# Kernel optimization log

Measured on AMD Instinct MI355X. Metric: run time of the kernel, lower is better.

## Reference

```python
import jax, jax.numpy as jnp
import numpy as np

B, T, C, H, W = 2, 2048, 2048, 16, 512
D = C // H  # head_dim = 128

def setup_inputs() -> dict:
    key = jax.random.key(0)
    k1, k2, k3 = jax.random.split(key, 3)
    x = jax.random.normal(k1, (B, T, C), dtype=jnp.float32)
    w_attn = jax.random.normal(k2, (C, 3 * C), dtype=jnp.float32) * 0.02
    w_proj = jax.random.normal(k3, (C, C), dtype=jnp.float32) * 0.02
    # standard RoPE tables: [T, D] with halves repeated
    inv_freq = 1.0 / (10000.0 ** (jnp.arange(0, D, 2, dtype=jnp.float32) / D))
    freqs = jnp.outer(jnp.arange(T, dtype=jnp.float32), inv_freq)  # [T, D/2]
    emb = jnp.concatenate([freqs, freqs], axis=-1)  # [T, D]
    return {"x": x, "freqs_cos": jnp.cos(emb), "freqs_sin": jnp.sin(emb),
            "w_attn": w_attn, "w_proj": w_proj}

def _rotate_half(t):
    return jnp.concatenate([-t[..., D // 2:], t[..., :D // 2]], axis=-1)

def reference(x, freqs_cos, freqs_sin, w_attn, w_proj):
    qkv = x @ w_attn  # [B,T,3C]
    q, k, v = jnp.split(qkv, 3, axis=-1)
    # [B,T,C] -> [B,H,T,D]
    q = q.reshape(B, T, H, D).transpose(0, 2, 1, 3)
    k = k.reshape(B, T, H, D).transpose(0, 2, 1, 3)
    v = v.reshape(B, T, H, D).transpose(0, 2, 1, 3)
    cos = freqs_cos[None, None, :, :]  # [1,1,T,D]
    sin = freqs_sin[None, None, :, :]
    q = q * cos + _rotate_half(q) * sin
    k = k * cos + _rotate_half(k) * sin
    scores = jnp.einsum('bhqd,bhkd->bhqk', q, k) / jnp.sqrt(jnp.float32(D))
    i = jnp.arange(T)[:, None]
    j = jnp.arange(T)[None, :]
    band = (j <= i) & (j > i - W)  # causal sliding window of width W
    scores = jnp.where(band[None, None, :, :], scores, -jnp.inf)
    att = jax.nn.softmax(scores, axis=-1)
    y = jnp.einsum('bhqk,bhkd->bhqd', att, v)
    y = y.transpose(0, 2, 1, 3).reshape(B, T, C)
    return y @ w_proj
```

## Files before the change

### kernel.cpp

```cpp
#include <hip/hip_runtime.h>
#include <stdint.h>

#define B_ 2
#define T_ 2048
#define C_ 2048
#define H_ 16
#define D_ 128
#define W_ 512
#define M_ (B_*T_)
#define N1_ (3*C_)

typedef short bf16x8 __attribute__((ext_vector_type(8)));
typedef unsigned short u16x8 __attribute__((ext_vector_type(8)));
typedef float f32x4 __attribute__((ext_vector_type(4)));

#define SGB __builtin_amdgcn_sched_group_barrier

__device__ __forceinline__ unsigned short f2bf(float f) {
  union { float f; unsigned u; } v; v.f = f;
  unsigned r = v.u + 0x7fffu + ((v.u >> 16) & 1u);
  return (unsigned short)(r >> 16);
}
__device__ __forceinline__ float bf2f(unsigned short b) {
  union { unsigned u; float f; } v; v.u = ((unsigned)b) << 16;
  return v.f;
}

__device__ __forceinline__ void gload_lds16(const void* g, void* l) {
  __builtin_amdgcn_global_load_lds((const __attribute__((address_space(1))) void*)g,
                                   (__attribute__((address_space(3))) void*)l, 16, 0, 0);
}

__global__ void k_cvt(const float* __restrict__ s, unsigned short* __restrict__ d, int n) {
  int i = (blockIdx.x * blockDim.x + threadIdx.x) * 8;
  if (i >= n) return;
  float4 a = *(const float4*)(s + i);
  float4 b = *(const float4*)(s + i + 4);
  u16x8 o;
  o[0]=f2bf(a.x); o[1]=f2bf(a.y); o[2]=f2bf(a.z); o[3]=f2bf(a.w);
  o[4]=f2bf(b.x); o[5]=f2bf(b.y); o[6]=f2bf(b.z); o[7]=f2bf(b.w);
  *(u16x8*)(d + i) = o;
}

__global__ void k_tcvt(const float* __restrict__ s, unsigned short* __restrict__ d, int R, int Cc) {
  __shared__ float tile[32][33];
  int c0 = blockIdx.x * 32, r0 = blockIdx.y * 32;
  int tx = threadIdx.x & 31, ty = threadIdx.x >> 5;
  #pragma unroll
  for (int j = 0; j < 32; j += 8) tile[ty + j][tx] = s[(size_t)(r0 + ty + j) * Cc + c0 + tx];
  __syncthreads();
  #pragma unroll
  for (int j = 0; j < 32; j += 8) d[(size_t)(c0 + ty + j) * R + r0 + tx] = f2bf(tile[tx][ty + j]);
}

template<int ROWS>
__device__ __forceinline__ void stage_half(const unsigned short* __restrict__ gbase,
                                           int row0, int K, int kt, int kh,
                                           unsigned short* region, int tid, int sw) {
  const char* gsrc = (const char*)(gbase + (size_t)row0 * K + kt * 64 + kh * 32);
  {
    int o = tid * 16, s = o ^ sw;
    gload_lds16(gsrc + (size_t)(s >> 6) * (K * 2) + (s & 63), (char*)region + o);
  }
  if (ROWS == 256) {
    int o = (512 + tid) * 16, s = o ^ sw;
    gload_lds16(gsrc + (size_t)(s >> 6) * (K * 2) + (s & 63), (char*)region + o);
  }
}

template<int BN, bool F32OUT>
__global__ __launch_bounds__(512, 2) void k_gemm8(const unsigned short* __restrict__ A,
                                                  const unsigned short* __restrict__ Bt,
                                                  void* __restrict__ Cp,
                                                  int Ntot, int K) {
  constexpr int NBF = BN / 64;
  constexpr int BROWS = (BN == 256) ? 256 : 128;
  __shared__ unsigned short As[2][2][256 * 32];
  __shared__ unsigned short Bs[2][2][BN * 32];
  const int tid = threadIdx.x, lane = tid & 63, wv = tid >> 6;
  const int wm = wv >> 2, wn = wv & 3;
  const int lr = lane & 15, lg = lane >> 4;
  const int sw = tid & 32;
  const int fofs = lr * 64 + ((lg * 16) ^ ((lr & 8) << 2));
  const int aoff = wm * 128 * 64 + fofs;
  const int boff = wn * (BN / 4) * 64 + fofs;

  const int nwg = gridDim.x;
  const int nbx = Ntot / BN;
  const int q = nwg >> 3, r = nwg & 7;
  const int xcd = blockIdx.x & 7, off = blockIdx.x >> 3;
  const int bid = (xcd < r ? xcd * (q + 1) : r * (q + 1) + (xcd - r) * q) + off;
  const int bm0 = (bid / nbx) << 8;
  const int bn0 = (bid % nbx) * BN;

  f32x4 acc[8][NBF];
  #pragma unroll
  for (int i = 0; i < 8; ++i)
    #pragma unroll
    for (int j = 0; j < NBF; ++j)
      #pragma unroll
      for (int e = 0; e < 4; ++e) acc[i][j][e] = 0.f;

  const int NT = K >> 6;

  stage_half<256  >(A,  bm0, K, 0, 0, As[0][0], tid, sw);
  stage_half<BROWS>(Bt, bn0, K, 0, 0, Bs[0][0], tid, sw);
  stage_half<BROWS>(Bt, bn0, K, 0, 1, Bs[0][1], tid, sw);
  stage_half<256  >(A,  bm0, K, 0, 1, As[0][1], tid, sw);
  stage_half<BROWS>(Bt, bn0, K, 1, 0, Bs[1][0], tid, sw);
  stage_half<256  >(A,  bm0, K, 1, 0, As[1][0], tid, sw);
  stage_half<BROWS>(Bt, bn0, K, 1, 1, Bs[1][1], tid, sw);
  asm volatile("s_waitcnt vmcnt(4)" ::: "memory");
  __builtin_amdgcn_s_barrier();

  bf16x8 Xa[4], Xb[NBF], Ya[4];
  #pragma unroll
  for (int j = 0; j < NBF; ++j) Xb[j] = *(const bf16x8*)((const char*)Bs[0][0] + boff + j * 1024);
  #pragma unroll
  for (int i = 0; i < 4; ++i) Xa[i] = *(const bf16x8*)((const char*)As[0][0] + aoff + i * 1024);

  #pragma unroll 2
  for (int t = 0; t < NT; ++t) {
    const int p = t & 1;
    const char* Ar0 = (const char*)As[p][0];
    const char* Ar1 = (const char*)As[p][1];
    const char* Br1 = (const char*)Bs[p][1];
    const char* ArN = (const char*)As[p ^ 1][0];
    const char* BrN = (const char*)Bs[p ^ 1][0];

    asm volatile("s_waitcnt lgkmcnt(0)" ::: "memory");
    __builtin_amdgcn_sched_barrier(0);
    __builtin_amdgcn_s_setprio(1);
    #pragma unroll
    for (int j = 0; j < NBF; ++j)
      #pragma unroll
      for (int i = 0; i < 4; ++i)
        acc[i][j] = __builtin_amdgcn_mfma_f32_16x16x32_bf16(Xa[i], Xb[j], acc[i][j], 0, 0, 0);
    #pragma unroll
    for (int i = 0; i < 4; ++i) Ya[i] = *(const bf16x8*)(Ar0 + aoff + (i + 4) * 1024);
    #pragma unroll
    for (int g = 0; g < 2 * NBF; ++g) { SGB(0x8, 2, 0); if (g < 4) SGB(0x100, 1, 0); }
    __builtin_amdgcn_s_setprio(0);
    if (t + 1 < NT) stage_half<256>(A, bm0, K, t + 1, 1, As[p ^ 1][1], tid, sw);
    __builtin_amdgcn_s_barrier();

    asm volatile("s_waitcnt lgkmcnt(0)" ::: "memory");
    __builtin_amdgcn_sched_barrier(0);
    __builtin_amdgcn_s_setprio(1);
    #pragma unroll
    for (int j = 0; j < NBF; ++j)
      #pragma unroll
      for (int i = 0; i < 4; ++i)
        acc[i + 4][j] = __builtin_amdgcn_mfma_f32_16x16x32_bf16(Ya[i], Xb[j], acc[i + 4][j], 0, 0, 0);
    #pragma unroll
    for (int i = 0; i < 4; ++i) Xa[i] = *(const bf16x8*)(Ar1 + aoff + i * 1024);
    #pragma unroll
    for (int j = 0; j < NBF; ++j) Xb[j] = *(const bf16x8*)(Br1 + boff + j * 1024);
    #pragma unroll
    for (int g = 0; g < 2 * NBF; ++g) { SGB(0x8, 2, 0); if (g < 4 + NBF) SGB(0x100, 1, 0); }
    if (4 + NBF > 2 * NBF) SGB(0x100, 4 + NBF - 2 * NBF, 0);
    __builtin_amdgcn_s_setprio(0);
    if (t + 2 < NT) stage_half<BROWS>(Bt, bn0, K, t + 2, 0, Bs[p][0], tid, sw);
    __builtin_amdgcn_s_barrier();

    asm volatile("s_waitcnt lgkmcnt(0)" ::: "memory");
    __builtin_amdgcn_sched_barrier(0);
    __builtin_amdgcn_s_setprio(1);
    #pragma unroll
    for (int j = 0; j < NBF; ++j)
      #pragma unroll
      for (int i = 0; i < 4; ++i)
        acc[i][j] = __builtin_amdgcn_mfma_f32_16x16x32_bf16(Xa[i], Xb[j], acc[i][j], 0, 0, 0);
    #pragma unroll
    for (int i = 0; i < 4; ++i) Ya[i] = *(const bf16x8*)(Ar1 + aoff + (i + 4) * 1024);
    #pragma unroll
    for (int g = 0; g < 2 * NBF; ++g) { SGB(0x8, 2, 0); if (g < 4) SGB(0x100, 1, 0); }
    __builtin_amdgcn_s_setprio(0);
    if (t + 2 < NT) stage_half<256>(A, bm0, K, t + 2, 0, As[p][0], tid, sw);
    __builtin_amdgcn_s_barrier();

    asm volatile("s_waitcnt lgkmcnt(0)" ::: "memory");
    __builtin_amdgcn_sched_barrier(0);
    if (t < NT - 2) {
      if (BN == 256) asm volatile("s_waitcnt vmcnt(4)" ::: "memory");
      else           asm volatile("s_waitcnt vmcnt(3)" ::: "memory");
    } else {
      asm volatile("s_waitcnt vmcnt(0)" ::: "memory");
    }
    __builtin_amdgcn_sched_barrier(0);
    __builtin_amdgcn_s_setprio(1);
    #pragma unroll
    for (int j = 0; j < NBF; ++j)
      #pragma unroll
      for (int i = 0; i < 4; ++i)
        acc[i + 4][j] = __builtin_amdgcn_mfma_f32_16x16x32_bf16(Ya[i], Xb[j], acc[i + 4][j], 0, 0, 0);
    #pragma unroll
    for (int i = 0; i < 4; ++i) Xa[i] = *(const bf16x8*)(ArN + aoff + i * 1024);
    #pragma unroll
    for (int j = 0; j < NBF; ++j) Xb[j] = *(const bf16x8*)(BrN + boff + j * 1024);
    #pragma unroll
    for (int g = 0; g < 2 * NBF; ++g) { SGB(0x8, 2, 0); if (g < 4 + NBF) SGB(0x100, 1, 0); }
    if (4 + NBF > 2 * NBF) SGB(0x100, 4 + NBF - 2 * NBF, 0);
    __builtin_amdgcn_s_setprio(0);
    if (t + 2 < NT) stage_half<BROWS>(Bt, bn0, K, t + 2, 1, Bs[p][1], tid, sw);
    __builtin_amdgcn_s_barrier();
  }
  asm volatile("s_waitcnt lgkmcnt(0)" ::: "memory");

  #pragma unroll
  for (int i = 0; i < 8; ++i)
    #pragma unroll
    for (int j = 0; j < NBF; ++j) {
      int m = bm0 + wm * 128 + i * 16 + lg * 4;
      int n = bn0 + wn * (BN / 4) + j * 16 + lr;
      #pragma unroll
      for (int e = 0; e < 4; ++e) {
        if (F32OUT) ((float*)Cp)[(size_t)(m + e) * Ntot + n] = acc[i][j][e];
        else ((unsigned short*)Cp)[(size_t)(m + e) * Ntot + n] = f2bf(acc[i][j][e]);
      }
    }
}

__global__ __launch_bounds__(256) void k_reorg(const unsigned short* __restrict__ qkv,
                        const float* __restrict__ fcos, const float* __restrict__ fsin,
                        unsigned short* __restrict__ q_r, unsigned short* __restrict__ k_r,
                        unsigned short* __restrict__ v_t) {
  const int bh = blockIdx.x, b = bh >> 4, h = bh & 15;
  const int t0 = blockIdx.y * 64;
  const int tid = threadIdx.x;
  __shared__ unsigned short vt[64][136];
  #pragma unroll
  for (int p = 0; p < 4; ++p) {
    int idx = p * 256 + tid;
    int tl = idx >> 4, sg = idx & 15;
    int t = t0 + tl, d0 = sg * 8;
    float sgn = (d0 < 64) ? -1.f : 1.f;
    float4 c0v = *(const float4*)(fcos + t * D_ + d0);
    float4 c1v = *(const float4*)(fcos + t * D_ + d0 + 4);
    float4 s0v = *(const float4*)(fsin + t * D_ + d0);
    float4 s1v = *(const float4*)(fsin + t * D_ + d0 + 4);
    float cs[8] = {c0v.x,c0v.y,c0v.z,c0v.w,c1v.x,c1v.y,c1v.z,c1v.w};
    float sn[8] = {s0v.x,s0v.y,s0v.z,s0v.w,s1v.x,s1v.y,s1v.z,s1v.w};
    #pragma unroll
    for (int w = 0; w < 2; ++w) {
      const unsigned short* src = qkv + (size_t)(b*T_ + t) * N1_ + w*C_ + h*D_;
      u16x8 a  = *(const u16x8*)(src + d0);
      u16x8 pr = *(const u16x8*)(src + (d0 ^ 64));
      u16x8 o;
      #pragma unroll
      for (int e = 0; e < 8; ++e)
        o[e] = f2bf(bf2f(a[e]) * cs[e] + sgn * bf2f(pr[e]) * sn[e]);
      unsigned short* dst = (w ? k_r : q_r) + (size_t)((b*H_ + h)*T_ + t) * D_ + d0;
      *(u16x8*)dst = o;
    }
    const unsigned short* vsrc = qkv + (size_t)(b*T_ + t) * N1_ + 2*C_ + h*D_ + d0;
    *(u16x8*)&vt[tl][d0] = *(const u16x8*)vsrc;
  }
  __syncthreads();
  #pragma unroll
  for (int p = 0; p < 4; ++p) {
    int idx = p * 256 + tid;
    int sg = idx & 7, d = idx >> 3;
    u16x8 o;
    #pragma unroll
    for (int e = 0; e < 8; ++e) o[e] = vt[sg*8 + e][d];
    *(u16x8*)(v_t + (size_t)((b*H_ + h)*D_ + d) * T_ + t0 + sg*8) = o;
  }
}

__global__ __launch_bounds__(256) void k_attn(const unsigned short* __restrict__ q_r,
                       const unsigned short* __restrict__ k_r,
                       const unsigned short* __restrict__ v_t,
                       unsigned short* __restrict__ y) {
  const int bh = blockIdx.x, b = bh >> 4, h = bh & 15;
  const int q0 = blockIdx.y * 64;
  const int tid = threadIdx.x, lane = tid & 63, wv = tid >> 6;
  const int lr = lane & 15, lg = lane >> 4;

  __shared__ unsigned short Ks[64][136];
  __shared__ unsigned short Vs[128][72];
  __shared__ unsigned short Ps[4][16][80];

  const size_t bhT = (size_t)(b*H_ + h) * T_;
  const unsigned short* qbase = q_r + (bhT + q0 + wv*16 + lr) * D_;
  bf16x8 qf[4];
  #pragma unroll
  for (int kk = 0; kk < 4; ++kk) qf[kk] = *(const bf16x8*)(qbase + kk*32 + lg*8);

  f32x4 o[8];
  #pragma unroll
  for (int i = 0; i < 8; ++i)
    #pragma unroll
    for (int e = 0; e < 4; ++e) o[i][e] = 0.f;
  float m_run[4], l_sum[4];
  #pragma unroll
  for (int e = 0; e < 4; ++e) { m_run[e] = -1e30f; l_sum[e] = 0.f; }

  const int i_min = q0 + wv*16, i_max = i_min + 15;
  int kt_lo = q0 - (W_ - 1); if (kt_lo < 0) kt_lo = 0; kt_lo &= ~63;
  const float scale = 0.08838834764831845f;

  for (int kt = kt_lo; kt < q0 + 64; kt += 64) {
    #pragma unroll
    for (int p = 0; p < 4; ++p) {
      int idx = p*256 + tid;
      int row = idx >> 4, sg = idx & 15;
      *(u16x8*)&Ks[row][sg*8] = *(const u16x8*)(k_r + (bhT + kt + row) * D_ + sg*8);
    }
    #pragma unroll
    for (int p = 0; p < 4; ++p) {
      int idx = p*256 + tid;
      int d = idx >> 3, sg = idx & 7;
      *(u16x8*)&Vs[d][sg*8] = *(const u16x8*)(v_t + ((size_t)(b*H_+h)*D_ + d) * T_ + kt + sg*8);
    }
    __syncthreads();

    if (kt <= i_max && kt + 63 >= i_min - (W_ - 1)) {
      f32x4 s[4];
      #pragma unroll
      for (int ct = 0; ct < 4; ++ct)
        #pragma unroll
        for (int e = 0; e < 4; ++e) s[ct][e] = 0.f;
      #pragma unroll
      for (int kk = 0; kk < 4; ++kk) {
        #pragma unroll
        for (int ct = 0; ct < 4; ++ct) {
          bf16x8 kf = *(const bf16x8*)((const char*)&Ks[ct*16 + lr][0] + kk*64 + lg*16);
          s[ct] = __builtin_amdgcn_mfma_f32_16x16x32_bf16(qf[kk], kf, s[ct], 0, 0, 0);
        }
      }
      #pragma unroll
      for (int e = 0; e < 4; ++e) {
        int i = i_min + lg*4 + e;
        float sv[4];
        float rm = -1e30f;
        #pragma unroll
        for (int ct = 0; ct < 4; ++ct) {
          int j = kt + ct*16 + lr;
          bool ok = (j <= i) && (j > i - W_);
          sv[ct] = ok ? s[ct][e] * scale : -1e30f;
          rm = fmaxf(rm, sv[ct]);
        }
        #pragma unroll
        for (int msk = 1; msk < 16; msk <<= 1) rm = fmaxf(rm, __shfl_xor(rm, msk));
        float mnew = fmaxf(m_run[e], rm);
        float fac = __expf(m_run[e] - mnew);
        float rs = 0.f;
        #pragma unroll
        for (int ct = 0; ct < 4; ++ct) {
          float pv = (sv[ct] > -1e29f) ? __expf(sv[ct] - mnew) : 0.f;
          rs += pv;
          Ps[wv][lg*4 + e][ct*16 + lr] = f2bf(pv);
        }
        #pragma unroll
        for (int msk = 1; msk < 16; msk <<= 1) rs += __shfl_xor(rs, msk);
        l_sum[e] = l_sum[e] * fac + rs;
        m_run[e] = mnew;
        #pragma unroll
        for (int nt = 0; nt < 8; ++nt) o[nt][e] *= fac;
      }
      asm volatile("s_waitcnt lgkmcnt(0)" ::: "memory");
      #pragma unroll
      for (int kk = 0; kk < 2; ++kk) {
        bf16x8 pf = *(const bf16x8*)((const char*)&Ps[wv][lr][0] + kk*64 + lg*16);
        #pragma unroll
        for (int nt = 0; nt < 8; ++nt) {
          bf16x8 vf = *(const bf16x8*)((const char*)&Vs[nt*16 + lr][0] + kk*64 + lg*16);
          o[nt] = __builtin_amdgcn_mfma_f32_16x16x32_bf16(pf, vf, o[nt], 0, 0, 0);
        }
      }
    }
    __syncthreads();
  }

  #pragma unroll
  for (int nt = 0; nt < 8; ++nt) {
    #pragma unroll
    for (int e = 0; e < 4; ++e) {
      int t = q0 + wv*16 + lg*4 + e;
      int d = nt*16 + lr;
      y[(size_t)(b*T_ + t) * C_ + h*D_ + d] = f2bf(o[nt][e] / l_sum[e]);
    }
  }
}

extern "C" void kernel_launch(void* const* d_in, const int* in_sizes, int n_in,
                              void* d_out, int out_size, void* d_ws, size_t ws_size,
                              hipStream_t stream) {
  const float* x      = (const float*)d_in[0];
  const float* fcos   = (const float*)d_in[1];
  const float* fsin   = (const float*)d_in[2];
  const float* w_attn = (const float*)d_in[3];
  const float* w_proj = (const float*)d_in[4];
  float* out = (float*)d_out;

  char* ws = (char*)d_ws;
  unsigned short* x_bf = (unsigned short*)(ws);
  unsigned short* wa_t = (unsigned short*)(ws + 16777216ull);
  unsigned short* wp_t = (unsigned short*)(ws + 41943040ull);
  unsigned short* qkv  = (unsigned short*)(ws + 50331648ull);
  unsigned short* q_r  = (unsigned short*)(ws + 100663296ull);
  unsigned short* k_r  = (unsigned short*)(ws + 117440512ull);
  unsigned short* v_t  = (unsigned short*)(ws + 134217728ull);
  unsigned short* y_bf = x_bf;

  k_cvt<<<dim3(4096), dim3(256), 0, stream>>>(x, x_bf, M_*C_);
  k_tcvt<<<dim3(192, 64), dim3(256), 0, stream>>>(w_attn, wa_t, C_, N1_);
  k_tcvt<<<dim3(64, 64), dim3(256), 0, stream>>>(w_proj, wp_t, C_, C_);
  k_gemm8<256, false><<<dim3(384), dim3(512), 0, stream>>>(x_bf, wa_t, qkv, N1_, C_);
  k_reorg<<<dim3(32, 32), dim3(256), 0, stream>>>(qkv, fcos, fsin, q_r, k_r, v_t);
  k_attn<<<dim3(32, 32), dim3(256), 0, stream>>>(q_r, k_r, v_t, y_bf);
  k_gemm8<128, true><<<dim3(256), dim3(512), 0, stream>>>(y_bf, wp_t, out, C_, C_);
}
```

Before: 304.3 us.

## Restructure GEMM fragment double-buffering and enlarge attention tiles with swizzled LDS

```diff
diff --git a/kernel.cpp b/kernel.cpp
--- a/kernel.cpp
+++ b/kernel.cpp
@@ -14,7 +14,7 @@
 typedef unsigned short u16x8 __attribute__((ext_vector_type(8)));
 typedef float f32x4 __attribute__((ext_vector_type(4)));
 
-#define SGB __builtin_amdgcn_sched_group_barrier
+#define SB() __builtin_amdgcn_sched_barrier(0)
 
 __device__ __forceinline__ unsigned short f2bf(float f) {
   union { float f; unsigned u; } v; v.f = f;
@@ -75,6 +75,8 @@
                                                   int Ntot, int K) {
   constexpr int NBF = BN / 64;
   constexpr int BROWS = (BN == 256) ? 256 : 128;
+  constexpr int V0 = (BN == 256) ? 6 : 4;
+  constexpr int V1 = (BN == 256) ? 4 : 3;
   __shared__ unsigned short As[2][2][256 * 32];
   __shared__ unsigned short Bs[2][2][BN * 32];
   const int tid = threadIdx.x, lane = tid & 63, wv = tid >> 6;
@@ -110,14 +112,15 @@
   stage_half<BROWS>(Bt, bn0, K, 1, 0, Bs[1][0], tid, sw);
   stage_half<256  >(A,  bm0, K, 1, 0, As[1][0], tid, sw);
   stage_half<BROWS>(Bt, bn0, K, 1, 1, Bs[1][1], tid, sw);
-  asm volatile("s_waitcnt vmcnt(4)" ::: "memory");
+  if (BN == 256) asm volatile("s_waitcnt vmcnt(10)" ::: "memory");
+  else           asm volatile("s_waitcnt vmcnt(7)"  ::: "memory");
   __builtin_amdgcn_s_barrier();
 
-  bf16x8 Xa[4], Xb[NBF], Ya[4];
-  #pragma unroll
-  for (int j = 0; j < NBF; ++j) Xb[j] = *(const bf16x8*)((const char*)Bs[0][0] + boff + j * 1024);
-  #pragma unroll
-  for (int i = 0; i < 4; ++i) Xa[i] = *(const bf16x8*)((const char*)As[0][0] + aoff + i * 1024);
+  bf16x8 Pf[4], Qf[4], Xf[NBF], Yf[NBF];
+  #pragma unroll
+  for (int i = 0; i < 4; ++i) Pf[i] = *(const bf16x8*)((const char*)As[0][0] + aoff + i * 1024);
+  #pragma unroll
+  for (int j = 0; j < NBF; ++j) Xf[j] = *(const bf16x8*)((const char*)Bs[0][0] + boff + j * 1024);
 
   #pragma unroll 2
   for (int t = 0; t < NT; ++t) {
@@ -128,79 +131,74 @@
     const char* ArN = (const char*)As[p ^ 1][0];
     const char* BrN = (const char*)Bs[p ^ 1][0];
 
-    asm volatile("s_waitcnt lgkmcnt(0)" ::: "memory");
-    __builtin_amdgcn_sched_barrier(0);
+    asm volatile("s_waitcnt lgkmcnt(0)" ::: "memory"); SB();
+    if (t < NT - 2) { if (BN==256) asm volatile("s_waitcnt vmcnt(6)" ::: "memory");
+                      else         asm volatile("s_waitcnt vmcnt(4)" ::: "memory"); }
+    else            asm volatile("s_waitcnt vmcnt(0)" ::: "memory");
+    SB();
+    #pragma unroll
+    for (int i = 0; i < 4; ++i) Qf[i] = *(const bf16x8*)(Ar0 + aoff + (i + 4) * 1024);
+    SB();
     __builtin_amdgcn_s_setprio(1);
     #pragma unroll
-    for (int j = 0; j < NBF; ++j)
-      #pragma unroll
-      for (int i = 0; i < 4; ++i)
-        acc[i][j] = __builtin_amdgcn_mfma_f32_16x16x32_bf16(Xa[i], Xb[j], acc[i][j], 0, 0, 0);
-    #pragma unroll
-    for (int i = 0; i < 4; ++i) Ya[i] = *(const bf16x8*)(Ar0 + aoff + (i + 4) * 1024);
-    #pragma unroll
-    for (int g = 0; g < 2 * NBF; ++g) { SGB(0x8, 2, 0); if (g < 4) SGB(0x100, 1, 0); }
+    for (int i = 0; i < 4; ++i)
+      #pragma unroll
+      for (int j = 0; j < NBF; ++j)
+        acc[i][j] = __builtin_amdgcn_mfma_f32_16x16x32_bf16(Pf[i], Xf[j], acc[i][j], 0, 0, 0);
     __builtin_amdgcn_s_setprio(0);
     if (t + 1 < NT) stage_half<256>(A, bm0, K, t + 1, 1, As[p ^ 1][1], tid, sw);
     __builtin_amdgcn_s_barrier();
 
-    asm volatile("s_waitcnt lgkmcnt(0)" ::: "memory");
-    __builtin_amdgcn_sched_barrier(0);
+    asm volatile("s_waitcnt lgkmcnt(0)" ::: "memory"); SB();
+    if (t < NT - 2) { if (BN==256) asm volatile("s_waitcnt vmcnt(4)" ::: "memory");
+                      else         asm volatile("s_waitcnt vmcnt(3)" ::: "memory"); }
+    else            asm volatile("s_waitcnt vmcnt(0)" ::: "memory");
+    SB();
+    #pragma unroll
+    for (int i = 0; i < 4; ++i) Pf[i] = *(const bf16x8*)(Ar1 + aoff + i * 1024);
+    #pragma unroll
+    for (int j = 0; j < NBF; ++j) Yf[j] = *(const bf16x8*)(Br1 + boff + j * 1024);
+    SB();
     __builtin_amdgcn_s_setprio(1);
     #pragma unroll
-    for (int j = 0; j < NBF; ++j)
-      #pragma unroll
-      for (int i = 0; i < 4; ++i)
-        acc[i + 4][j] = __builtin_amdgcn_mfma_f32_16x16x32_bf16(Ya[i], Xb[j], acc[i + 4][j], 0, 0, 0);
-    #pragma unroll
-    for (int i = 0; i < 4; ++i) Xa[i] = *(const bf16x8*)(Ar1 + aoff + i * 1024);
-    #pragma unroll
-    for (int j = 0; j < NBF; ++j) Xb[j] = *(const bf16x8*)(Br1 + boff + j * 1024);
-    #pragma unroll
-    for (int g = 0; g < 2 * NBF; ++g) { SGB(0x8, 2, 0); if (g < 4 + NBF) SGB(0x100, 1, 0); }
-    if (4 + NBF > 2 * NBF) SGB(0x100, 4 + NBF - 2 * NBF, 0);
+    for (int i = 0; i < 4; ++i)
+      #pragma unroll
+      for (int j = 0; j < NBF; ++j)
+        acc[i + 4][j] = __builtin_amdgcn_mfma_f32_16x16x32_bf16(Qf[i], Xf[j], acc[i + 4][j], 0, 0, 0);
     __builtin_amdgcn_s_setprio(0);
     if (t + 2 < NT) stage_half<BROWS>(Bt, bn0, K, t + 2, 0, Bs[p][0], tid, sw);
     __builtin_amdgcn_s_barrier();
 
-    asm volatile("s_waitcnt lgkmcnt(0)" ::: "memory");
-    __builtin_amdgcn_sched_barrier(0);
+    asm volatile("s_waitcnt lgkmcnt(0)" ::: "memory"); SB();
+    #pragma unroll
+    for (int i = 0; i < 4; ++i) Qf[i] = *(const bf16x8*)(Ar1 + aoff + (i + 4) * 1024);
+    if (t + 1 < NT) {
+      #pragma unroll
+      for (int j = 0; j < NBF; ++j) Xf[j] = *(const bf16x8*)(BrN + boff + j * 1024);
+    }
+    SB();
     __builtin_amdgcn_s_setprio(1);
     #pragma unroll
-    for (int j = 0; j < NBF; ++j)
-      #pragma unroll
-      for (int i = 0; i < 4; ++i)
-        acc[i][j] = __builtin_amdgcn_mfma_f32_16x16x32_bf16(Xa[i], Xb[j], acc[i][j], 0, 0, 0);
-    #pragma unroll
-    for (int i = 0; i < 4; ++i) Ya[i] = *(const bf16x8*)(Ar1 + aoff + (i + 4) * 1024);
-    #pragma unroll
-    for (int g = 0; g < 2 * NBF; ++g) { SGB(0x8, 2, 0); if (g < 4) SGB(0x100, 1, 0); }
+    for (int i = 0; i < 4; ++i)
+      #pragma unroll
+      for (int j = 0; j < NBF; ++j)
+        acc[i][j] = __builtin_amdgcn_mfma_f32_16x16x32_bf16(Pf[i], Yf[j], acc[i][j], 0, 0, 0);
     __builtin_amdgcn_s_setprio(0);
     if (t + 2 < NT) stage_half<256>(A, bm0, K, t + 2, 0, As[p][0], tid, sw);
     __builtin_amdgcn_s_barrier();
 
-    asm volatile("s_waitcnt lgkmcnt(0)" ::: "memory");
-    __builtin_amdgcn_sched_barrier(0);
-    if (t < NT - 2) {
-      if (BN == 256) asm volatile("s_waitcnt vmcnt(4)" ::: "memory");
-      else           asm volatile("s_waitcnt vmcnt(3)" ::: "memory");
-    } else {
-      asm volatile("s_waitcnt vmcnt(0)" ::: "memory");
-    }
-    __builtin_amdgcn_sched_barrier(0);
+    asm volatile("s_waitcnt lgkmcnt(0)" ::: "memory"); SB();
+    if (t + 1 < NT) {
+      #pragma unroll
+      for (int i = 0; i < 4; ++i) Pf[i] = *(const bf16x8*)(ArN + aoff + i * 1024);
+    }
+    SB();
     __builtin_amdgcn_s_setprio(1);
     #pragma unroll
-    for (int j = 0; j < NBF; ++j)
-      #pragma unroll
-      for (int i = 0; i < 4; ++i)
-        acc[i + 4][j] = __builtin_amdgcn_mfma_f32_16x16x32_bf16(Ya[i], Xb[j], acc[i + 4][j], 0, 0, 0);
-    #pragma unroll
-    for (int i = 0; i < 4; ++i) Xa[i] = *(const bf16x8*)(ArN + aoff + i * 1024);
-    #pragma unroll
-    for (int j = 0; j < NBF; ++j) Xb[j] = *(const bf16x8*)(BrN + boff + j * 1024);
-    #pragma unroll
-    for (int g = 0; g < 2 * NBF; ++g) { SGB(0x8, 2, 0); if (g < 4 + NBF) SGB(0x100, 1, 0); }
-    if (4 + NBF > 2 * NBF) SGB(0x100, 4 + NBF - 2 * NBF, 0);
+    for (int i = 0; i < 4; ++i)
+      #pragma unroll
+      for (int j = 0; j < NBF; ++j)
+        acc[i + 4][j] = __builtin_amdgcn_mfma_f32_16x16x32_bf16(Qf[i], Yf[j], acc[i + 4][j], 0, 0, 0);
     __builtin_amdgcn_s_setprio(0);
     if (t + 2 < NT) stage_half<BROWS>(Bt, bn0, K, t + 2, 1, Bs[p][1], tid, sw);
     __builtin_amdgcn_s_barrier();
@@ -268,20 +266,21 @@
   }
 }
 
-__global__ __launch_bounds__(256) void k_attn(const unsigned short* __restrict__ q_r,
+__global__ __launch_bounds__(512) void k_attn(const unsigned short* __restrict__ q_r,
                        const unsigned short* __restrict__ k_r,
                        const unsigned short* __restrict__ v_t,
                        unsigned short* __restrict__ y) {
   const int bh = blockIdx.x, b = bh >> 4, h = bh & 15;
-  const int q0 = blockIdx.y * 64;
+  const int q0 = blockIdx.y * 128;
   const int tid = threadIdx.x, lane = tid & 63, wv = tid >> 6;
   const int lr = lane & 15, lg = lane >> 4;
 
-  __shared__ unsigned short Ks[64][136];
-  __shared__ unsigned short Vs[128][72];
-  __shared__ unsigned short Ps[4][16][80];
+  __shared__ unsigned short Ks[64 * 128];
+  __shared__ unsigned short Vs[128 * 64];
+  __shared__ unsigned short Ps[8 * 16 * 64];
 
   const size_t bhT = (size_t)(b*H_ + h) * T_;
+  const size_t bhD = (size_t)(b*H_ + h) * D_;
   const unsigned short* qbase = q_r + (bhT + q0 + wv*16 + lr) * D_;
   bf16x8 qf[4];
   #pragma unroll
@@ -300,18 +299,22 @@
   int kt_lo = q0 - (W_ - 1); if (kt_lo < 0) kt_lo = 0; kt_lo &= ~63;
   const float scale = 0.08838834764831845f;
 
-  for (int kt = kt_lo; kt < q0 + 64; kt += 64) {
-    #pragma unroll
-    for (int p = 0; p < 4; ++p) {
-      int idx = p*256 + tid;
-      int row = idx >> 4, sg = idx & 15;
-      *(u16x8*)&Ks[row][sg*8] = *(const u16x8*)(k_r + (bhT + kt + row) * D_ + sg*8);
-    }
-    #pragma unroll
-    for (int p = 0; p < 4; ++p) {
-      int idx = p*256 + tid;
+  unsigned short* Ps_w = Ps + wv * 1024;
+
+  for (int kt = kt_lo; kt < q0 + 128; kt += 64) {
+    #pragma unroll
+    for (int c = 0; c < 2; ++c) {
+      int idx = c*512 + tid;
+      int row = idx >> 4, cb = idx & 15;
+      int cbs = cb ^ ((row & 7) << 1);
+      *(u16x8*)&Ks[row*128 + cbs*8] = *(const u16x8*)(k_r + (bhT + kt + row) * D_ + cb*8);
+    }
+    #pragma unroll
+    for (int c = 0; c < 2; ++c) {
+      int idx = c*512 + tid;
       int d = idx >> 3, sg = idx & 7;
-      *(u16x8*)&Vs[d][sg*8] = *(const u16x8*)(v_t + ((size_t)(b*H_+h)*D_ + d) * T_ + kt + sg*8);
+      int cbs = sg ^ (d & 7);
+      *(u16x8*)&Vs[d*64 + cbs*8] = *(const u16x8*)(v_t + (bhD + d) * T_ + kt + sg*8);
     }
     __syncthreads();
 
@@ -325,47 +328,59 @@
       for (int kk = 0; kk < 4; ++kk) {
         #pragma unroll
         for (int ct = 0; ct < 4; ++ct) {
-          bf16x8 kf = *(const bf16x8*)((const char*)&Ks[ct*16 + lr][0] + kk*64 + lg*16);
+          bf16x8 kf = *(const bf16x8*)&Ks[(ct*16 + lr)*128 + ((kk*4 + lg) ^ ((lr & 7) << 1))*8];
           s[ct] = __builtin_amdgcn_mfma_f32_16x16x32_bf16(qf[kk], kf, s[ct], 0, 0, 0);
         }
       }
+      float sv[4][4], mnew[4];
+      int grow = 0;
       #pragma unroll
       for (int e = 0; e < 4; ++e) {
         int i = i_min + lg*4 + e;
-        float sv[4];
         float rm = -1e30f;
         #pragma unroll
         for (int ct = 0; ct < 4; ++ct) {
           int j = kt + ct*16 + lr;
           bool ok = (j <= i) && (j > i - W_);
-          sv[ct] = ok ? s[ct][e] * scale : -1e30f;
-          rm = fmaxf(rm, sv[ct]);
+          sv[e][ct] = ok ? s[ct][e] * scale : -1e30f;
+          rm = fmaxf(rm, sv[e][ct]);
         }
         #pragma unroll
         for (int msk = 1; msk < 16; msk <<= 1) rm = fmaxf(rm, __shfl_xor(rm, msk));
-        float mnew = fmaxf(m_run[e], rm);
-        float fac = __expf(m_run[e] - mnew);
+        mnew[e] = fmaxf(m_run[e], rm);
+        grow |= (mnew[e] > m_run[e]) ? 1 : 0;
+      }
+      if (__any(grow)) {
+        #pragma unroll
+        for (int e = 0; e < 4; ++e) {
+          float fac = __expf(m_run[e] - mnew[e]);
+          l_sum[e] *= fac;
+          m_run[e] = mnew[e];
+          #pragma unroll
+          for (int nt = 0; nt < 8; ++nt) o[nt][e] *= fac;
+        }
+      }
+      #pragma unroll
+      for (int e = 0; e < 4; ++e) {
+        int prow = lg*4 + e;
         float rs = 0.f;
         #pragma unroll
         for (int ct = 0; ct < 4; ++ct) {
-          float pv = (sv[ct] > -1e29f) ? __expf(sv[ct] - mnew) : 0.f;
+          float pv = (sv[e][ct] > -1e29f) ? __expf(sv[e][ct] - m_run[e]) : 0.f;
           rs += pv;
-          Ps[wv][lg*4 + e][ct*16 + lr] = f2bf(pv);
+          Ps_w[prow*64 + ((ct*2 + (lr >> 3)) ^ (prow & 7))*8 + (lr & 7)] = f2bf(pv);
         }
         #pragma unroll
         for (int msk = 1; msk < 16; msk <<= 1) rs += __shfl_xor(rs, msk);
-        l_sum[e] = l_sum[e] * fac + rs;
-        m_run[e] = mnew;
-        #pragma unroll
-        for (int nt = 0; nt < 8; ++nt) o[nt][e] *= fac;
-      }
-      asm volatile("s_waitcnt lgkmcnt(0)" ::: "memory");
+        l_sum[e] += rs;
+      }
+      asm volatile("s_waitcnt lgkmcnt(0)" ::: "memory"); SB();
       #pragma unroll
       for (int kk = 0; kk < 2; ++kk) {
-        bf16x8 pf = *(const bf16x8*)((const char*)&Ps[wv][lr][0] + kk*64 + lg*16);
+        bf16x8 pf = *(const bf16x8*)&Ps_w[lr*64 + ((kk*4 + lg) ^ (lr & 7))*8];
         #pragma unroll
         for (int nt = 0; nt < 8; ++nt) {
-          bf16x8 vf = *(const bf16x8*)((const char*)&Vs[nt*16 + lr][0] + kk*64 + lg*16);
+          bf16x8 vf = *(const bf16x8*)&Vs[(nt*16 + lr)*64 + ((kk*4 + lg) ^ (lr & 7))*8];
           o[nt] = __builtin_amdgcn_mfma_f32_16x16x32_bf16(pf, vf, o[nt], 0, 0, 0);
         }
       }
@@ -409,6 +424,6 @@
   k_tcvt<<<dim3(64, 64), dim3(256), 0, stream>>>(w_proj, wp_t, C_, C_);
   k_gemm8<256, false><<<dim3(384), dim3(512), 0, stream>>>(x_bf, wa_t, qkv, N1_, C_);
   k_reorg<<<dim3(32, 32), dim3(256), 0, stream>>>(qkv, fcos, fsin, q_r, k_r, v_t);
-  k_attn<<<dim3(32, 32), dim3(256), 0, stream>>>(q_r, k_r, v_t, y_bf);
+  k_attn<<<dim3(32, 16), dim3(512), 0, stream>>>(q_r, k_r, v_t, y_bf);
   k_gemm8<128, true><<<dim3(256), dim3(512), 0, stream>>>(y_bf, wp_t, out, C_, C_);
 }
```

New measurement: 315.5 us. +3.7%, slower.
